# Kernel tuning notes

Measured on AMD Instinct MI355X. Metric: run time of the kernel, lower is better.

Reference implementation:

```python
import jax, jax.numpy as jnp
import numpy as np

N = 8192
E = 262144
SLOPE = 0.2  # PyG GATConv default leaky_relu negative_slope


def gat_conv(x, src, dst, W, a_src, a_dst, b):
    # x: [N, Fin]; src/dst: [E'] (self-loops already appended)
    h = x @ W                                   # [N, Fout]
    alpha_s = h @ a_src                         # [N]
    alpha_d = h @ a_dst                         # [N]
    e = jax.nn.leaky_relu(alpha_s[src] + alpha_d[dst], SLOPE)  # [E']
    # segment softmax over incoming edges of each dst node
    m = jax.ops.segment_max(e, dst, num_segments=N)
    e = jnp.exp(e - m[dst])
    denom = jax.ops.segment_sum(e, dst, num_segments=N)
    alpha = e / (denom[dst] + 1e-16)
    out = jax.ops.segment_sum(alpha[:, None] * h[src], dst, num_segments=N)
    return out + b


def setup_inputs() -> dict:
    key = jax.random.key(0)
    ks = jax.random.split(key, 8)
    x = jnp.eye(N, dtype=jnp.float32)  # source uses identity node features
    edge_index = jax.random.randint(ks[0], (2, E), 0, N, dtype=jnp.int64)
    s1 = 1.0 / np.sqrt(N)
    s2 = 1.0 / np.sqrt(256)
    return {
        "x": x,
        "edge_index": edge_index,
        "W1": jax.random.normal(ks[1], (N, 256), jnp.float32) * s1,
        "att_src1": jax.random.normal(ks[2], (256,), jnp.float32) * s2,
        "att_dst1": jax.random.normal(ks[3], (256,), jnp.float32) * s2,
        "b1": jnp.zeros((256,), jnp.float32),
        "W2": jax.random.normal(ks[4], (256, 128), jnp.float32) * s2,
        "att_src2": jax.random.normal(ks[5], (128,), jnp.float32) * (1.0 / np.sqrt(128)),
        "att_dst2": jax.random.normal(ks[6], (128,), jnp.float32) * (1.0 / np.sqrt(128)),
        "b2": jnp.zeros((128,), jnp.float32),
    }


def reference(x, edge_index, W1, att_src1, att_dst1, b1, W2, att_src2, att_dst2, b2):
    # PyG GATConv adds self-loops by default
    loops = jnp.arange(N, dtype=edge_index.dtype)
    src = jnp.concatenate([edge_index[0], loops])
    dst = jnp.concatenate([edge_index[1], loops])
    h = gat_conv(x, src, dst, W1, att_src1, att_dst1, b1)
    h = jax.nn.relu(h)
    h = gat_conv(h, src, dst, W2, att_src2, att_dst2, b2)
    z = jnp.tanh(h)                       # [N, 128]
    adj_recon = jax.nn.sigmoid(z @ z.T)   # [N, N]
    return (adj_recon, z)
```

## Files before the change

kernel.cpp:

```cpp
#include <hip/hip_runtime.h>
#include <hip/hip_bf16.h>


#define NN    8192
#define EBASE 262144
#define ETOT  (EBASE + NN)

typedef __bf16 bf16x8 __attribute__((ext_vector_type(8)));
typedef float  f32x4  __attribute__((ext_vector_type(4)));
typedef float  f32x2  __attribute__((ext_vector_type(2)));

__device__ __forceinline__ float bf2f(unsigned short u) {
  return __uint_as_float(((unsigned int)u) << 16);
}
__device__ __forceinline__ unsigned short f2bf(float f) {
  unsigned int u = __float_as_uint(f);
  return (unsigned short)((u + 0x7FFFu + ((u >> 16) & 1u)) >> 16);
}


__global__ void prep_hist_kernel(const float* __restrict__ W1, const float* __restrict__ asrc,
                                 const float* __restrict__ adst, unsigned short* __restrict__ w1b,
                                 float* __restrict__ al_s, float* __restrict__ al_d,
                                 const float* __restrict__ W2, unsigned short* __restrict__ w2f,
                                 const int* __restrict__ ei, int* __restrict__ deg) {
  if (blockIdx.x < NN / 4) {
    int wave = blockIdx.x * 4 + (threadIdx.x >> 6);
    int lane = threadIdx.x & 63;
    f32x4 v = *(const f32x4*)(W1 + (size_t)wave * 256 + lane * 4);
    f32x4 s4 = *(const f32x4*)(asrc + lane * 4);
    f32x4 d4 = *(const f32x4*)(adst + lane * 4);
    float ss = v[0] * s4[0] + v[1] * s4[1] + v[2] * s4[2] + v[3] * s4[3];
    float sd = v[0] * d4[0] + v[1] * d4[1] + v[2] * d4[2] + v[3] * d4[3];
#pragma unroll
    for (int o = 32; o; o >>= 1) { ss += __shfl_down(ss, o); sd += __shfl_down(sd, o); }
    ushort4 b;
    b.x = f2bf(v[0]); b.y = f2bf(v[1]); b.z = f2bf(v[2]); b.w = f2bf(v[3]);
    *(ushort4*)(w1b + (size_t)wave * 256 + lane * 4) = b;
    if (lane == 0) { al_s[wave] = ss; al_d[wave] = sd; }
  } else if (blockIdx.x < NN / 4 + 16) {
    int t = (blockIdx.x - NN / 4) * 256 + threadIdx.x;
    int lane = t & 63;
    int c = (t >> 6) & 7;
    int kk = t >> 9;
    int col = c * 16 + (lane & 15);
    int kbase = kk * 32 + (lane >> 4) * 8;
    unsigned short v[8];
#pragma unroll
    for (int j = 0; j < 8; ++j) v[j] = f2bf(W2[(size_t)(kbase + j) * 128 + col]);
    ushort4 lo, hi;
    lo.x = v[0]; lo.y = v[1]; lo.z = v[2]; lo.w = v[3];
    hi.x = v[4]; hi.y = v[5]; hi.z = v[6]; hi.w = v[7];
    *(ushort4*)(w2f + (size_t)t * 8) = lo;
    *(ushort4*)(w2f + (size_t)t * 8 + 4) = hi;
  } else {
    int e = (blockIdx.x - NN / 4 - 16) * 256 + threadIdx.x;
    if (e >= ETOT) return;
    int d = (e < EBASE) ? ei[EBASE + e] : (e - EBASE);
    atomicAdd(&deg[d], 1);
  }
}

__global__ void scan_kernel(const int* __restrict__ deg, int* __restrict__ offs,
                            int* __restrict__ cur) {
  __shared__ int part[1024];
  int t = threadIdx.x;
  int loc[8];
  int s = 0;
#pragma unroll
  for (int j = 0; j < 8; ++j) { loc[j] = deg[t * 8 + j]; s += loc[j]; }
  part[t] = s;
  __syncthreads();
  for (int o = 1; o < 1024; o <<= 1) {
    int v = (t >= o) ? part[t - o] : 0;
    __syncthreads();
    part[t] += v;
    __syncthreads();
  }
  int base = t ? part[t - 1] : 0;
#pragma unroll
  for (int j = 0; j < 8; ++j) { offs[t * 8 + j] = base; cur[t * 8 + j] = base; base += loc[j]; }
  if (t == 1023) offs[NN] = base;
}

__global__ void scatter_kernel(const int* __restrict__ ei, int* __restrict__ cur,
                               int* __restrict__ ssrc) {
  int e = blockIdx.x * 256 + threadIdx.x;
  if (e >= ETOT) return;
  int sv = (e < EBASE) ? ei[e] : (e - EBASE);
  int dv = (e < EBASE) ? ei[EBASE + e] : (e - EBASE);
  int pos = atomicAdd(&cur[dv], 1);
  ssrc[pos] = sv;
}


template <int F, int ACT>
__global__ __launch_bounds__(256) void agg_kernel(
    const int* __restrict__ offs, const int* __restrict__ ssrc,
    const unsigned short* __restrict__ hb, const float* __restrict__ as_,
    const float* __restrict__ ad_, const float* __restrict__ bias,
    unsigned short* __restrict__ outb, float* __restrict__ z,
    unsigned short* __restrict__ zb) {
  constexpr int VPL = F / 64;
  int d = blockIdx.x * 4 + (threadIdx.x >> 6);
  int lane = threadIdx.x & 63;
  int beg = offs[d];
  int deg = offs[d + 1] - beg;
  float adv = ad_[d];
  float accA[VPL] = {}, accB[VPL] = {}, accC[VPL] = {}, accD[VPL] = {};
  float inv;

  if (deg <= 64) {
    int s_reg = 0;
    float p_reg = 0.f;
    if (lane < deg) {
      s_reg = ssrc[beg + lane];
      float t = as_[s_reg] + adv;
      t = (t >= 0.f) ? t : 0.2f * t;
      p_reg = __expf(t);
    }
    float lsum = p_reg;
#pragma unroll
    for (int o = 32; o; o >>= 1) lsum += __shfl_xor(lsum, o);
    inv = 1.f / (lsum + 1e-16f);
    int i = 0;
    for (; i + 4 <= deg; i += 4) {
      int s0 = __shfl(s_reg, i), s1 = __shfl(s_reg, i + 1);
      int s2 = __shfl(s_reg, i + 2), s3 = __shfl(s_reg, i + 3);
      float p0 = __shfl(p_reg, i), p1 = __shfl(p_reg, i + 1);
      float p2 = __shfl(p_reg, i + 2), p3 = __shfl(p_reg, i + 3);
      if constexpr (VPL == 4) {
        ushort4 u0 = *(const ushort4*)(hb + (size_t)s0 * F + lane * 4);
        ushort4 u1 = *(const ushort4*)(hb + (size_t)s1 * F + lane * 4);
        ushort4 u2 = *(const ushort4*)(hb + (size_t)s2 * F + lane * 4);
        ushort4 u3 = *(const ushort4*)(hb + (size_t)s3 * F + lane * 4);
        accA[0] += p0 * bf2f(u0.x); accA[1] += p0 * bf2f(u0.y);
        accA[2] += p0 * bf2f(u0.z); accA[3] += p0 * bf2f(u0.w);
        accB[0] += p1 * bf2f(u1.x); accB[1] += p1 * bf2f(u1.y);
        accB[2] += p1 * bf2f(u1.z); accB[3] += p1 * bf2f(u1.w);
        accC[0] += p2 * bf2f(u2.x); accC[1] += p2 * bf2f(u2.y);
        accC[2] += p2 * bf2f(u2.z); accC[3] += p2 * bf2f(u2.w);
        accD[0] += p3 * bf2f(u3.x); accD[1] += p3 * bf2f(u3.y);
        accD[2] += p3 * bf2f(u3.z); accD[3] += p3 * bf2f(u3.w);
      } else {
        ushort2 u0 = *(const ushort2*)(hb + (size_t)s0 * F + lane * 2);
        ushort2 u1 = *(const ushort2*)(hb + (size_t)s1 * F + lane * 2);
        ushort2 u2 = *(const ushort2*)(hb + (size_t)s2 * F + lane * 2);
        ushort2 u3 = *(const ushort2*)(hb + (size_t)s3 * F + lane * 2);
        accA[0] += p0 * bf2f(u0.x); accA[1] += p0 * bf2f(u0.y);
        accB[0] += p1 * bf2f(u1.x); accB[1] += p1 * bf2f(u1.y);
        accC[0] += p2 * bf2f(u2.x); accC[1] += p2 * bf2f(u2.y);
        accD[0] += p3 * bf2f(u3.x); accD[1] += p3 * bf2f(u3.y);
      }
    }
    for (; i < deg; ++i) {
      int si = __shfl(s_reg, i);
      float pi = __shfl(p_reg, i);
      if constexpr (VPL == 4) {
        ushort4 u = *(const ushort4*)(hb + (size_t)si * F + lane * 4);
        accA[0] += pi * bf2f(u.x); accA[1] += pi * bf2f(u.y);
        accA[2] += pi * bf2f(u.z); accA[3] += pi * bf2f(u.w);
      } else {
        ushort2 u = *(const ushort2*)(hb + (size_t)si * F + lane * 2);
        accA[0] += pi * bf2f(u.x); accA[1] += pi * bf2f(u.y);
      }
    }
  } else {
    float lsum = 0.f;
    for (int i = lane; i < deg; i += 64) {
      int s = ssrc[beg + i];
      float t = as_[s] + adv;
      t = (t >= 0.f) ? t : 0.2f * t;
      lsum += __expf(t);
    }
#pragma unroll
    for (int o = 32; o; o >>= 1) lsum += __shfl_xor(lsum, o);
    inv = 1.f / (lsum + 1e-16f);
    for (int i = 0; i < deg; ++i) {
      int s = ssrc[beg + i];
      float t = as_[s] + adv;
      t = (t >= 0.f) ? t : 0.2f * t;
      float pi = __expf(t);
      if constexpr (VPL == 4) {
        ushort4 u = *(const ushort4*)(hb + (size_t)s * F + lane * 4);
        accA[0] += pi * bf2f(u.x); accA[1] += pi * bf2f(u.y);
        accA[2] += pi * bf2f(u.z); accA[3] += pi * bf2f(u.w);
      } else {
        ushort2 u = *(const ushort2*)(hb + (size_t)s * F + lane * 2);
        accA[0] += pi * bf2f(u.x); accA[1] += pi * bf2f(u.y);
      }
    }
  }

  float r[VPL];
#pragma unroll
  for (int j = 0; j < VPL; ++j)
    r[j] = ((accA[j] + accB[j]) + (accC[j] + accD[j])) * inv + bias[lane * VPL + j];
  if constexpr (ACT == 0) {
    ushort4 st;
    st.x = f2bf(fmaxf(r[0], 0.f)); st.y = f2bf(fmaxf(r[1], 0.f));
    st.z = f2bf(fmaxf(r[2], 0.f)); st.w = f2bf(fmaxf(r[3], 0.f));
    *(ushort4*)(outb + (size_t)d * F + lane * 4) = st;
  } else {
    float z0 = tanhf(r[0]), z1 = tanhf(r[1]);
    f32x2 zf; zf[0] = z0; zf[1] = z1;
    __builtin_nontemporal_store(zf, (f32x2*)(z + (size_t)d * F + lane * 2));
    ushort2 zs; zs.x = f2bf(z0); zs.y = f2bf(z1);
    *(ushort2*)(zb + (size_t)d * F + lane * 2) = zs;
  }
}


__global__ __launch_bounds__(64) void gemm2m_kernel(const unsigned short* __restrict__ out1b,
                                                    const unsigned short* __restrict__ w2f,
                                                    const float* __restrict__ as2,
                                                    const float* __restrict__ ad2,
                                                    unsigned short* __restrict__ h2b,
                                                    float* __restrict__ al_s,
                                                    float* __restrict__ al_d) {
  int lane = threadIdx.x;
  int row0 = blockIdx.x * 16;
  int arow = row0 + (lane & 15);
  int kofs = (lane >> 4) * 8;
  f32x4 acc[8] = {};
#pragma unroll
  for (int kk = 0; kk < 8; ++kk) {
    bf16x8 a = *(const bf16x8*)(out1b + (size_t)arow * 256 + kk * 32 + kofs);
#pragma unroll
    for (int c = 0; c < 8; ++c) {
      bf16x8 b = *(const bf16x8*)(w2f + ((size_t)(kk * 8 + c) * 64 + lane) * 8);
      acc[c] = __builtin_amdgcn_mfma_f32_16x16x32_bf16(a, b, acc[c], 0, 0, 0);
    }
  }
  int rbase = row0 + (lane >> 4) * 4;
  int cbase = lane & 15;
  float vs[4] = {}, vd[4] = {};
#pragma unroll
  for (int c = 0; c < 8; ++c) {
    float sa = as2[c * 16 + cbase], da = ad2[c * 16 + cbase];
#pragma unroll
    for (int j = 0; j < 4; ++j) {
      float v = acc[c][j];
      h2b[(size_t)(rbase + j) * 128 + c * 16 + cbase] = f2bf(v);
      vs[j] += v * sa;
      vd[j] += v * da;
    }
  }
#pragma unroll
  for (int j = 0; j < 4; ++j) {
#pragma unroll
    for (int o = 1; o < 16; o <<= 1) {
      vs[j] += __shfl_xor(vs[j], o);
      vd[j] += __shfl_xor(vd[j], o);
    }
    if (cbase == 0) { al_s[rbase + j] = vs[j]; al_d[rbase + j] = vd[j]; }
  }
}


__global__ __launch_bounds__(256) void adj_kernel(const unsigned short* __restrict__ zb,
                                                  float* __restrict__ out) {
  int bid = blockIdx.x;
  int brow = bid >> 6, bcol = bid & 63;
  int tid = threadIdx.x;
  int wave = tid >> 6, lane = tid & 63;
  int wr = wave >> 1, wc = wave & 1;
  int rowbase = brow * 128 + wr * 64;
  int colbase = bcol * 128 + wc * 64;
  int lr = lane & 15;
  int ko = (lane >> 4) * 8;

  f32x4 acc[4][4] = {};
#pragma unroll
  for (int kk = 0; kk < 4; ++kk) {
    int k = kk * 32 + ko;
    bf16x8 a[4], b[4];
#pragma unroll
    for (int m = 0; m < 4; ++m)
      a[m] = *(const bf16x8*)(zb + (size_t)(rowbase + m * 16 + lr) * 128 + k);
#pragma unroll
    for (int n = 0; n < 4; ++n)
      b[n] = *(const bf16x8*)(zb + (size_t)(colbase + n * 16 + lr) * 128 + k);
#pragma unroll
    for (int m = 0; m < 4; ++m)
#pragma unroll
      for (int n = 0; n < 4; ++n)
        acc[m][n] = __builtin_amdgcn_mfma_f32_16x16x32_bf16(a[m], b[n], acc[m][n], 0, 0, 0);
  }

  int r0 = (lane >> 4) * 4;
  int c0 = lane & 15;
#pragma unroll
  for (int m = 0; m < 4; ++m) {
#pragma unroll
    for (int n = 0; n < 4; ++n) {
      int col = colbase + n * 16 + c0;
#pragma unroll
      for (int j = 0; j < 4; ++j) {
        int row = rowbase + m * 16 + r0 + j;
        float v = acc[m][n][j];
        out[(size_t)row * NN + col] = __builtin_amdgcn_rcpf(1.f + __expf(-v));
      }
    }
  }
}


extern "C" void kernel_launch(void* const* d_in, const int* in_sizes, int n_in,
                              void* d_out, int out_size, void* d_ws, size_t ws_size,
                              hipStream_t stream) {
  const int* ei = (const int*)d_in[1];
  const float* W1 = (const float*)d_in[2];
  const float* as1 = (const float*)d_in[3];
  const float* ad1 = (const float*)d_in[4];
  const float* b1 = (const float*)d_in[5];
  const float* W2 = (const float*)d_in[6];
  const float* as2 = (const float*)d_in[7];
  const float* ad2 = (const float*)d_in[8];
  const float* b2 = (const float*)d_in[9];

  float* adj = (float*)d_out;
  float* z = adj + (size_t)NN * NN;

  char* ws = (char*)d_ws;
  int* deg = (int*)(ws + 0x000000);
  int* offs = (int*)(ws + 0x010000);
  int* cur = (int*)(ws + 0x020000);
  int* ssrc = (int*)(ws + 0x030000);
  float* al_s1 = (float*)(ws + 0x140000);
  float* al_d1 = (float*)(ws + 0x148000);
  float* al_s2 = (float*)(ws + 0x150000);
  float* al_d2 = (float*)(ws + 0x158000);
  unsigned short* w1b = (unsigned short*)(ws + 0x160000);
  unsigned short* out1b = (unsigned short*)(ws + 0x560000);
  unsigned short* h2b = (unsigned short*)(ws + 0x960000);
  unsigned short* zb = (unsigned short*)(ws + 0xB60000);
  unsigned short* w2f = (unsigned short*)(ws + 0xD60000);

  (void)hipMemsetAsync(deg, 0, NN * sizeof(int), stream);

  int egrid = (ETOT + 255) / 256;
  prep_hist_kernel<<<NN / 4 + 16 + egrid, 256, 0, stream>>>(W1, as1, ad1, w1b, al_s1, al_d1,
                                                            W2, w2f, ei, deg);
  scan_kernel<<<1, 1024, 0, stream>>>(deg, offs, cur);
  scatter_kernel<<<egrid, 256, 0, stream>>>(ei, cur, ssrc);

  agg_kernel<256, 0><<<NN / 4, 256, 0, stream>>>(offs, ssrc, w1b, al_s1, al_d1, b1,
                                                 out1b, nullptr, nullptr);

  gemm2m_kernel<<<512, 64, 0, stream>>>(out1b, w2f, as2, ad2, h2b, al_s2, al_d2);
  agg_kernel<128, 1><<<NN / 4, 256, 0, stream>>>(offs, ssrc, h2b, al_s2, al_d2, b2,
                                                 nullptr, z, zb);

  adj_kernel<<<64 * 64, 256, 0, stream>>>(zb, adj);
}
```

Measured before the change: 488.0 us.

## Retile adjacency kernel and stage sigmoid output through LDS for coalesced stores

Reshapes the adj_kernel tile so each wave computes 16 rows by 256 columns instead of a 64x64 block, giving a 64x256 tile per block and a matching grid. Sigmoid results go into padded shared memory first, then each wave writes full contiguous rows with 16-byte vector stores. This targets the scattered 4-byte stores of the 256 MB fp32 output, which likely dominate the kernel. In exchange, each A fragment is reused less, more B loads are needed, and the block now uses about 66 KB of LDS, which may limit occupancy.

```diff
diff --git a/kernel.cpp b/kernel.cpp
--- a/kernel.cpp
+++ b/kernel.cpp
@@ -258,50 +258,50 @@
 }
 
 
+#define LSTR 260
+
 __global__ __launch_bounds__(256) void adj_kernel(const unsigned short* __restrict__ zb,
                                                   float* __restrict__ out) {
+  __shared__ float lds[4][16][LSTR];
   int bid = blockIdx.x;
-  int brow = bid >> 6, bcol = bid & 63;
-  int tid = threadIdx.x;
-  int wave = tid >> 6, lane = tid & 63;
-  int wr = wave >> 1, wc = wave & 1;
-  int rowbase = brow * 128 + wr * 64;
-  int colbase = bcol * 128 + wc * 64;
+  int brow = bid >> 5;
+  int bcol = bid & 31;
+  int wave = threadIdx.x >> 6, lane = threadIdx.x & 63;
+  int rowbase = brow * 64 + wave * 16;
+  int colw = bcol * 256;
   int lr = lane & 15;
   int ko = (lane >> 4) * 8;
 
-  f32x4 acc[4][4] = {};
+  f32x4 acc[16] = {};
 #pragma unroll
   for (int kk = 0; kk < 4; ++kk) {
     int k = kk * 32 + ko;
-    bf16x8 a[4], b[4];
-#pragma unroll
-    for (int m = 0; m < 4; ++m)
-      a[m] = *(const bf16x8*)(zb + (size_t)(rowbase + m * 16 + lr) * 128 + k);
-#pragma unroll
-    for (int n = 0; n < 4; ++n)
-      b[n] = *(const bf16x8*)(zb + (size_t)(colbase + n * 16 + lr) * 128 + k);
-#pragma unroll
-    for (int m = 0; m < 4; ++m)
-#pragma unroll
-      for (int n = 0; n < 4; ++n)
-        acc[m][n] = __builtin_amdgcn_mfma_f32_16x16x32_bf16(a[m], b[n], acc[m][n], 0, 0, 0);
+    bf16x8 a = *(const bf16x8*)(zb + (size_t)(rowbase + lr) * 128 + k);
+#pragma unroll
+    for (int n = 0; n < 16; ++n) {
+      bf16x8 b = *(const bf16x8*)(zb + (size_t)(colw + n * 16 + lr) * 128 + k);
+      acc[n] = __builtin_amdgcn_mfma_f32_16x16x32_bf16(a, b, acc[n], 0, 0, 0);
+    }
   }
 
   int r0 = (lane >> 4) * 4;
   int c0 = lane & 15;
 #pragma unroll
-  for (int m = 0; m < 4; ++m) {
-#pragma unroll
-    for (int n = 0; n < 4; ++n) {
-      int col = colbase + n * 16 + c0;
-#pragma unroll
-      for (int j = 0; j < 4; ++j) {
-        int row = rowbase + m * 16 + r0 + j;
-        float v = acc[m][n][j];
-        out[(size_t)row * NN + col] = __builtin_amdgcn_rcpf(1.f + __expf(-v));
-      }
-    }
+  for (int n = 0; n < 16; ++n) {
+#pragma unroll
+    for (int j = 0; j < 4; ++j) {
+      float v = acc[n][j];
+      lds[wave][r0 + j][n * 16 + c0] = __builtin_amdgcn_rcpf(1.f + __expf(-v));
+    }
+  }
+#pragma unroll
+  for (int r = 0; r < 16; ++r) {
+    f32x4 vv;
+    vv[0] = lds[wave][r][lane * 4 + 0];
+    vv[1] = lds[wave][r][lane * 4 + 1];
+    vv[2] = lds[wave][r][lane * 4 + 2];
+    vv[3] = lds[wave][r][lane * 4 + 3];
+    *(f32x4*)(out + (size_t)(rowbase + r) * NN + colw + lane * 4) = vv;
   }
 }
 
@@ -352,5 +352,5 @@
   agg_kernel<128, 1><<<NN / 4, 256, 0, stream>>>(offs, ssrc, h2b, al_s2, al_d2, b2,
                                                  nullptr, z, zb);
 
-  adj_kernel<<<64 * 64, 256, 0, stream>>>(zb, adj);
-}
+  adj_kernel<<<128 * 32, 256, 0, stream>>>(zb, adj);
+}
```

Measured after the change: 560.0 us. 1.15x slower.
